# Performance work log

Hardware: AMD Instinct MI355X
Metric: run time of the kernel (lower is better)

Reference implementation:

```python
import jax, jax.numpy as jnp
import numpy as np

B = 4096   # batch
I = 1024   # in_features
O = 1024   # out_features
N = 4      # LUT fan-in; table size 2**N = 16


def setup_inputs() -> dict:
    key = jax.random.key(0)
    k1, k2, k3 = jax.random.split(key, 3)
    return {
        "x": jax.random.normal(k1, (B, I), dtype=jnp.float32),
        # learnable mapping logits: (out_features, n, in_features)
        "mapping_logits": jax.random.normal(k2, (O, N, I), dtype=jnp.float32),
        # per-node LUT tables with 2**n corner values each
        "lut_tables": jax.random.normal(k3, (O, 2 ** N), dtype=jnp.float32),
    }


def reference(x, mapping_logits, lut_tables):
    # softmax-weighted input selection: (B,I) x (O,N,I) -> (B,O,N)
    w = jax.nn.softmax(mapping_logits, axis=-1)
    selected = jnp.einsum('bi,oni->bon', x, w)
    # BatchedLUTNodes: squash to [0,1], multilinear interpolation over 2**N corners
    s = jax.nn.sigmoid(selected)                      # (B,O,N)
    cw = jnp.ones(s.shape[:2] + (1,), dtype=s.dtype)  # corner weights, grows to (B,O,2**N)
    for j in range(N):                                # fixed small loop over fan-in
        sj = s[..., j][..., None]                     # (B,O,1)
        cw = jnp.concatenate([cw * (1.0 - sj), cw * sj], axis=-1)
    # weighted sum of per-node table entries -> (B,O)
    return jnp.einsum('boc,oc->bo', cw, lut_tables)
```

## Files before the change

kernel.cpp:

```cpp
#include <hip/hip_runtime.h>

#define B_DIM 4096
#define I_DIM 1024
#define O_DIM 1024
#define ON_DIM 4096
#define TILE_HALFS 4096

typedef _Float16 half8   __attribute__((ext_vector_type(8)));
typedef _Float16 half4_t __attribute__((ext_vector_type(4)));
typedef float    floatx16 __attribute__((ext_vector_type(16)));

__global__ __launch_bounds__(256)
void ltn_prep1(const float* __restrict__ logits, const float* __restrict__ x,
               float2* __restrict__ stats, _Float16* __restrict__ xt) {
  const int t = threadIdx.x;
  if (blockIdx.x < 1024) {
    const int lane = t & 63, wv = t >> 6;
    const int row = blockIdx.x * 4 + wv;
    const float4* src = (const float4*)(logits + (size_t)row * I_DIM);
    float4 v[4];
#pragma unroll
    for (int j = 0; j < 4; j++) v[j] = src[j * 64 + lane];
    float m = -1e30f;
#pragma unroll
    for (int j = 0; j < 4; j++)
      m = fmaxf(m, fmaxf(fmaxf(v[j].x, v[j].y), fmaxf(v[j].z, v[j].w)));
#pragma unroll
    for (int off = 1; off < 64; off <<= 1) m = fmaxf(m, __shfl_xor(m, off));
    float s = 0.0f;
#pragma unroll
    for (int j = 0; j < 4; j++) {
      s += __expf(v[j].x - m) + __expf(v[j].y - m)
         + __expf(v[j].z - m) + __expf(v[j].w - m);
    }
#pragma unroll
    for (int off = 1; off < 64; off <<= 1) s += __shfl_xor(s, off);
    if (lane == 0) stats[row] = make_float2(m, 1.0f / s);
  } else {
    const int bid = blockIdx.x - 1024;
    const int mb = bid >> 5, kt = bid & 31;
    const int nn = t >> 1, hf = t & 1;
    const int row = mb * 128 + nn;
    const float4* src = (const float4*)(x + (size_t)row * I_DIM + kt * 32 + hf * 16);
    const float4 a = src[0], b = src[1], c = src[2], d = src[3];
    half8 h0, h1;
    h0[0] = (_Float16)a.x; h0[1] = (_Float16)a.y; h0[2] = (_Float16)a.z; h0[3] = (_Float16)a.w;
    h0[4] = (_Float16)b.x; h0[5] = (_Float16)b.y; h0[6] = (_Float16)b.z; h0[7] = (_Float16)b.w;
    h1[0] = (_Float16)c.x; h1[1] = (_Float16)c.y; h1[2] = (_Float16)c.z; h1[3] = (_Float16)c.w;
    h1[4] = (_Float16)d.x; h1[5] = (_Float16)d.y; h1[6] = (_Float16)d.z; h1[7] = (_Float16)d.w;
    _Float16* base = xt + ((size_t)mb * 32 + kt) * TILE_HALFS + (hf * 2) * 1024 + nn * 8;
    *(half8*)base = h0;
    *(half8*)(base + 1024) = h1;
  }
}

__global__ __launch_bounds__(256)
void ltn_prep2(const float* __restrict__ logits, const float2* __restrict__ stats,
               _Float16* __restrict__ wt) {
  const int t  = threadIdx.x;
  const int nn = t >> 1, hf = t & 1;
  const int nb = blockIdx.x >> 5, kb = blockIdx.x & 31;
  const int row = nb * 128 + nn;
  const float2 st = stats[row];
  const float4* src = (const float4*)(logits + (size_t)row * I_DIM + kb * 32 + hf * 16);
  const float4 a = src[0], b = src[1], c = src[2], d = src[3];
  half8 h0, h1;
  h0[0] = (_Float16)(__expf(a.x - st.x) * st.y);
  h0[1] = (_Float16)(__expf(a.y - st.x) * st.y);
  h0[2] = (_Float16)(__expf(a.z - st.x) * st.y);
  h0[3] = (_Float16)(__expf(a.w - st.x) * st.y);
  h0[4] = (_Float16)(__expf(b.x - st.x) * st.y);
  h0[5] = (_Float16)(__expf(b.y - st.x) * st.y);
  h0[6] = (_Float16)(__expf(b.z - st.x) * st.y);
  h0[7] = (_Float16)(__expf(b.w - st.x) * st.y);
  h1[0] = (_Float16)(__expf(c.x - st.x) * st.y);
  h1[1] = (_Float16)(__expf(c.y - st.x) * st.y);
  h1[2] = (_Float16)(__expf(c.z - st.x) * st.y);
  h1[3] = (_Float16)(__expf(c.w - st.x) * st.y);
  h1[4] = (_Float16)(__expf(d.x - st.x) * st.y);
  h1[5] = (_Float16)(__expf(d.y - st.x) * st.y);
  h1[6] = (_Float16)(__expf(d.z - st.x) * st.y);
  h1[7] = (_Float16)(__expf(d.w - st.x) * st.y);
  _Float16* base = wt + ((size_t)nb * 32 + kb) * TILE_HALFS + (hf * 2) * 1024 + nn * 8;
  *(half8*)base = h0;
  *(half8*)(base + 1024) = h1;
}

__global__ __launch_bounds__(512, 4)
void ltn_gemm_lut(const _Float16* __restrict__ xt,
                  const _Float16* __restrict__ wt,
                  const float* __restrict__ lut,
                  float* __restrict__ out) {
  __shared__ _Float16 As[2][2][4][128][8];
  __shared__ _Float16 Bs[2][4][128][8];

  const int tid  = threadIdx.x;
  const int lane = tid & 63;
  const int wv   = tid >> 6;
  const int wr   = wv >> 1;
  const int wc   = wv & 1;
  const int mb   = blockIdx.x;
  const int nb   = blockIdx.y;
  const int l31  = lane & 31;
  const int lhi  = lane >> 5;

  const size_t baseA = (size_t)(mb * 2) * 32 * TILE_HALFS;
  const size_t baseB = (size_t)nb * 32 * TILE_HALFS;

  floatx16 acc[2][2];
#pragma unroll
  for (int i = 0; i < 2; i++)
#pragma unroll
    for (int j = 0; j < 2; j++) acc[i][j] = (floatx16)0.0f;

  auto stage = [&](int buf, int kt) {
#pragma unroll
    for (int s = 0; s < 3; s++) {
      const int c = wv * 3 + s;
      const _Float16* g;
      char* l;
      if (c < 16) {
        const int tl = c >> 3, sub = c & 7;
        g = xt + baseA + (size_t)(tl * 32 + kt) * TILE_HALFS + sub * 512 + lane * 8;
        l = (char*)&As[buf][0][0][0][0] + c * 1024;
      } else {
        const int sub = c - 16;
        g = wt + baseB + (size_t)kt * TILE_HALFS + sub * 512 + lane * 8;
        l = (char*)&Bs[buf][0][0][0] + sub * 1024;
      }
      __builtin_amdgcn_global_load_lds(
          (const __attribute__((address_space(1))) void*)g,
          (__attribute__((address_space(3))) void*)l, 16, 0, 0);
    }
  };

  auto compute = [&](int buf) {
#pragma unroll
    for (int s = 0; s < 2; s++) {
      const int kb = s * 2 + lhi;
      half8 af[2], bf[2];
#pragma unroll
      for (int tm = 0; tm < 2; tm++) {
        const int rr = wr * 2 + tm;
        af[tm] = *(const half8*)&As[buf][rr >> 2][kb][(rr & 3) * 32 + l31][0];
      }
#pragma unroll
      for (int tn = 0; tn < 2; tn++)
        bf[tn] = *(const half8*)&Bs[buf][kb][wc * 64 + tn * 32 + l31][0];
#pragma unroll
      for (int tm = 0; tm < 2; tm++)
#pragma unroll
        for (int tn = 0; tn < 2; tn++)
          acc[tm][tn] = __builtin_amdgcn_mfma_f32_32x32x16_f16(
              af[tm], bf[tn], acc[tm][tn], 0, 0, 0);
    }
  };

  stage(0, 0);
  int buf = 0;
  for (int kt = 0; kt < 32; kt++) {
    __syncthreads();
    if (kt + 1 < 32) stage(buf ^ 1, kt + 1);
    compute(buf);
    buf ^= 1;
  }

#pragma unroll
  for (int tn = 0; tn < 2; tn++) {
    const int o = (nb * 128 + wc * 64 + tn * 32 + l31) >> 2;
    const float4* lt4 = (const float4*)(lut + (size_t)o * 16);
    const float4 L0 = lt4[0], L1 = lt4[1], L2 = lt4[2], L3 = lt4[3];
#pragma unroll
    for (int tm = 0; tm < 2; tm++) {
#pragma unroll
      for (int r = 0; r < 16; r++) {
        const float v  = acc[tm][tn][r];
        const float sv = 1.0f / (1.0f + __expf(-v));
        const float s1 = __shfl_down(sv, 1);
        const float s2 = __shfl_down(sv, 2);
        const float s3 = __shfl_down(sv, 3);
        if ((lane & 3) == 0) {
          const float s0 = sv;
          const float a0 = L0.x + (L2.x - L0.x) * s3;
          const float a1 = L0.y + (L2.y - L0.y) * s3;
          const float a2 = L0.z + (L2.z - L0.z) * s3;
          const float a3 = L0.w + (L2.w - L0.w) * s3;
          const float a4 = L1.x + (L3.x - L1.x) * s3;
          const float a5 = L1.y + (L3.y - L1.y) * s3;
          const float a6 = L1.z + (L3.z - L1.z) * s3;
          const float a7 = L1.w + (L3.w - L1.w) * s3;
          const float b0 = a0 + (a4 - a0) * s2;
          const float b1 = a1 + (a5 - a1) * s2;
          const float b2 = a2 + (a6 - a2) * s2;
          const float b3 = a3 + (a7 - a3) * s2;
          const float c0 = b0 + (b2 - b0) * s1;
          const float c1 = b1 + (b3 - b1) * s1;
          const float res = c0 + (c1 - c0) * s0;
          const int row = mb * 256 + wr * 64 + tm * 32
                        + (r & 3) + 8 * (r >> 2) + 4 * lhi;
          out[(size_t)row * O_DIM + o] = res;
        }
      }
    }
  }
}

extern "C" void kernel_launch(void* const* d_in, const int* in_sizes, int n_in,
                              void* d_out, int out_size, void* d_ws, size_t ws_size,
                              hipStream_t stream) {
  const float* x      = (const float*)d_in[0];
  const float* logits = (const float*)d_in[1];
  const float* lut    = (const float*)d_in[2];
  float* out          = (float*)d_out;

  _Float16* wt = (_Float16*)d_ws;
  _Float16* xt = (_Float16*)d_ws + (size_t)ON_DIM * I_DIM;
  float2* stats = (float2*)d_out;

  ltn_prep1<<<2048, 256, 0, stream>>>(logits, x, stats, xt);
  ltn_prep2<<<1024, 256, 0, stream>>>(logits, stats, wt);
  dim3 grid(16, 32);
  ltn_gemm_lut<<<grid, 512, 0, stream>>>(xt, wt, lut, out);
}
```

Baseline: 138.6 us.

## Shrink GEMM tile to 128x128 and load B fragments directly into registers

The GEMM block tile drops from 256x128 with 512 threads to 128x128 with 256 threads, which doubles the grid to 32x32 blocks. The B operand no longer goes through LDS. Each wave loads its B fragments from global memory straight into registers, prefetched one k-step ahead, while A stays double-buffered in LDS. This is meant to cut LDS traffic and footprint and to raise occupancy and block count, at the cost of more global reads of B and of A per block, plus extra VGPRs for the prefetched fragments.

```diff
diff --git a/kernel.cpp b/kernel.cpp
--- a/kernel.cpp
+++ b/kernel.cpp
@@ -7,7 +7,6 @@
 #define TILE_HALFS 4096
 
 typedef _Float16 half8   __attribute__((ext_vector_type(8)));
-typedef _Float16 half4_t __attribute__((ext_vector_type(4)));
 typedef float    floatx16 __attribute__((ext_vector_type(16)));
 
 __global__ __launch_bounds__(256)
@@ -86,13 +85,12 @@
   *(half8*)(base + 1024) = h1;
 }
 
-__global__ __launch_bounds__(512, 4)
+__global__ __launch_bounds__(256, 4)
 void ltn_gemm_lut(const _Float16* __restrict__ xt,
                   const _Float16* __restrict__ wt,
                   const float* __restrict__ lut,
                   float* __restrict__ out) {
-  __shared__ _Float16 As[2][2][4][128][8];
-  __shared__ _Float16 Bs[2][4][128][8];
+  __shared__ _Float16 As[2][4][128][8];
 
   const int tid  = threadIdx.x;
   const int lane = tid & 63;
@@ -104,8 +102,9 @@
   const int l31  = lane & 31;
   const int lhi  = lane >> 5;
 
-  const size_t baseA = (size_t)(mb * 2) * 32 * TILE_HALFS;
-  const size_t baseB = (size_t)nb * 32 * TILE_HALFS;
+  const _Float16* baseA = xt + (size_t)mb * 32 * TILE_HALFS;
+  const _Float16* pB = wt + (size_t)nb * 32 * TILE_HALFS
+                     + lhi * 1024 + (wc * 64 + l31) * 8;
 
   floatx16 acc[2][2];
 #pragma unroll
@@ -113,55 +112,50 @@
 #pragma unroll
     for (int j = 0; j < 2; j++) acc[i][j] = (floatx16)0.0f;
 
-  auto stage = [&](int buf, int kt) {
-#pragma unroll
-    for (int s = 0; s < 3; s++) {
-      const int c = wv * 3 + s;
-      const _Float16* g;
-      char* l;
-      if (c < 16) {
-        const int tl = c >> 3, sub = c & 7;
-        g = xt + baseA + (size_t)(tl * 32 + kt) * TILE_HALFS + sub * 512 + lane * 8;
-        l = (char*)&As[buf][0][0][0][0] + c * 1024;
-      } else {
-        const int sub = c - 16;
-        g = wt + baseB + (size_t)kt * TILE_HALFS + sub * 512 + lane * 8;
-        l = (char*)&Bs[buf][0][0][0] + sub * 1024;
-      }
+  auto stageA = [&](int buf, int kt) {
+#pragma unroll
+    for (int s = 0; s < 2; s++) {
+      const int c = wv * 2 + s;
+      const _Float16* g = baseA + (size_t)kt * TILE_HALFS + c * 512 + lane * 8;
       __builtin_amdgcn_global_load_lds(
           (const __attribute__((address_space(1))) void*)g,
-          (__attribute__((address_space(3))) void*)l, 16, 0, 0);
+          (__attribute__((address_space(3))) void*)((char*)&As[buf][0][0][0] + c * 1024),
+          16, 0, 0);
     }
   };
-
-  auto compute = [&](int buf) {
-#pragma unroll
-    for (int s = 0; s < 2; s++) {
-      const int kb = s * 2 + lhi;
-      half8 af[2], bf[2];
-#pragma unroll
-      for (int tm = 0; tm < 2; tm++) {
-        const int rr = wr * 2 + tm;
-        af[tm] = *(const half8*)&As[buf][rr >> 2][kb][(rr & 3) * 32 + l31][0];
-      }
-#pragma unroll
-      for (int tn = 0; tn < 2; tn++)
-        bf[tn] = *(const half8*)&Bs[buf][kb][wc * 64 + tn * 32 + l31][0];
-#pragma unroll
-      for (int tm = 0; tm < 2; tm++)
-#pragma unroll
-        for (int tn = 0; tn < 2; tn++)
-          acc[tm][tn] = __builtin_amdgcn_mfma_f32_32x32x16_f16(
-              af[tm], bf[tn], acc[tm][tn], 0, 0, 0);
-    }
+  auto loadB = [&](int kt, half8* bf) {
+    const half8* p = (const half8*)(pB + (size_t)kt * TILE_HALFS);
+    bf[0] = p[0];
+    bf[1] = p[32];
+    bf[2] = p[256];
+    bf[3] = p[288];
   };
 
-  stage(0, 0);
+  half8 bfc[4], bfn[4];
+  stageA(0, 0);
+  loadB(0, bfc);
   int buf = 0;
   for (int kt = 0; kt < 32; kt++) {
     __syncthreads();
-    if (kt + 1 < 32) stage(buf ^ 1, kt + 1);
-    compute(buf);
+    if (kt + 1 < 32) { stageA(buf ^ 1, kt + 1); loadB(kt + 1, bfn); }
+#pragma unroll
+    for (int s = 0; s < 2; s++) {
+      const int kb = s * 2 + lhi;
+      half8 af[2];
+#pragma unroll
+      for (int tm = 0; tm < 2; tm++) {
+        const int rr = wr * 2 + tm;
+        af[tm] = *(const half8*)&As[buf][kb][rr * 32 + l31][0];
+      }
+#pragma unroll
+      for (int tm = 0; tm < 2; tm++)
+#pragma unroll
+        for (int tn = 0; tn < 2; tn++)
+          acc[tm][tn] = __builtin_amdgcn_mfma_f32_32x32x16_f16(
+              af[tm], bfc[s * 2 + tn], acc[tm][tn], 0, 0, 0);
+    }
+#pragma unroll
+    for (int q = 0; q < 4; q++) bfc[q] = bfn[q];
     buf ^= 1;
   }
 
@@ -196,7 +190,7 @@
           const float c0 = b0 + (b2 - b0) * s1;
           const float c1 = b1 + (b3 - b1) * s1;
           const float res = c0 + (c1 - c0) * s0;
-          const int row = mb * 256 + wr * 64 + tm * 32
+          const int row = mb * 128 + wr * 64 + tm * 32
                         + (r & 3) + 8 * (r >> 2) + 4 * lhi;
           out[(size_t)row * O_DIM + o] = res;
         }
@@ -219,6 +213,6 @@
 
   ltn_prep1<<<2048, 256, 0, stream>>>(logits, x, stats, xt);
   ltn_prep2<<<1024, 256, 0, stream>>>(logits, stats, wt);
-  dim3 grid(16, 32);
-  ltn_gemm_lut<<<grid, 512, 0, stream>>>(xt, wt, lut, out);
-}
+  dim3 grid(32, 32);
+  ltn_gemm_lut<<<grid, 256, 0, stream>>>(xt, wt, lut, out);
+}
```

Result: no change. 140.3 us (+1.2%).
